# Optimization experiments

Measured on AMD Instinct MI355X. Metric: run time of the kernel, lower is better.

Reference implementation:

```python
import math
import jax, jax.numpy as jnp
import numpy as np

H = 16          # num attention heads
D = 64          # head dim
BUCKETS = 256   # position_buckets
MAX_POS = 512   # max_relative_positions
ATT_SPAN = BUCKETS  # pos_ebd_size A
SCALE_FACTOR = 3    # 1 + len(['c2p','p2c'])


def _log_bucket(rel):
    # log-bucketed relative positions (DeBERTa-v2 _make_log_bucket_position)
    mid = BUCKETS // 2
    rel = jnp.clip(rel, -MAX_POS + 1, MAX_POS - 1)
    sign = jnp.sign(rel).astype(jnp.float32)
    abs_pos = jnp.maximum(jnp.abs(rel), 1)
    log_base = math.log((MAX_POS - 1) / mid)
    log_pos = jnp.ceil(jnp.log(abs_pos.astype(jnp.float32) / mid) / log_base * (mid - 1)) + mid
    bucket = jnp.where(abs_pos < mid, abs_pos.astype(jnp.float32), log_pos) * sign
    return bucket.astype(jnp.int32)


def _rel_pos(q_len, k_len):
    q = jnp.arange(q_len, dtype=jnp.int32)
    k = jnp.arange(k_len, dtype=jnp.int32)
    return _log_bucket(q[:, None] - k[None, :])  # (Q, K)


def setup_inputs() -> dict:
    key = jax.random.key(0)
    ks = jax.random.split(key, 6)
    B, S, Hd = 4, 1024, 1024
    std = 0.02
    return {
        "hidden_states": jax.random.normal(ks[0], (B, S, Hd), jnp.float32),
        "rel_embeddings": jax.random.normal(ks[1], (2 * ATT_SPAN, Hd), jnp.float32) * std,
        "Wq": jax.random.normal(ks[2], (Hd, H * D), jnp.float32) * std,
        "bq": jnp.zeros((H * D,), jnp.float32),
        "Wk": jax.random.normal(ks[3], (Hd, H * D), jnp.float32) * std,
        "bk": jnp.zeros((H * D,), jnp.float32),
        "Wv": jax.random.normal(ks[4], (Hd, H * D), jnp.float32) * std,
        "bv": jnp.zeros((H * D,), jnp.float32),
    }


def reference(hidden_states, rel_embeddings, Wq, bq, Wk, bk, Wv, bv):
    B, S, Hd = hidden_states.shape
    A2 = 2 * ATT_SPAN

    def heads(x):  # (B,S,H*D) -> (B,H,S,D)
        return x.reshape(B, S, H, D).transpose(0, 2, 1, 3)

    q = heads(hidden_states @ Wq + bq)
    k = heads(hidden_states @ Wk + bk)
    v = heads(hidden_states @ Wv + bv)

    scale = math.sqrt(D * SCALE_FACTOR)
    scores = jnp.einsum('bhqd,bhkd->bhqk', q, k) / scale  # (B,H,S,S)

    rel = _rel_pos(S, S)  # (S,S) int32 bucketed relative ids
    # share_att_key=True: pos key/query use key_proj/query_proj
    pos_k = (rel_embeddings @ Wk + bk).reshape(A2, H, D).transpose(1, 0, 2)  # (H,2A,D)
    pos_q = (rel_embeddings @ Wq + bq).reshape(A2, H, D).transpose(1, 0, 2)  # (H,2A,D)

    # c2p: content->position
    c2p = jnp.einsum('bhqd,hkd->bhqk', q, pos_k)  # (B,H,S,2A)
    c2p_idx = jnp.clip(rel + ATT_SPAN, 0, A2 - 1)  # (S,S)
    c2p = jnp.take_along_axis(c2p, jnp.broadcast_to(c2p_idx[None, None], (B, H, S, S)), axis=-1) / scale

    # p2c: position->content
    p2c = jnp.einsum('bhkd,hqd->bhkq', k, pos_q)  # (B,H,S,2A)
    p2c_idx = jnp.clip(-rel + ATT_SPAN, 0, A2 - 1)  # (S,S)
    p2c = jnp.take_along_axis(p2c, jnp.broadcast_to(p2c_idx[None, None], (B, H, S, S)), axis=-1)
    p2c = jnp.swapaxes(p2c, -1, -2) / scale

    probs = jax.nn.softmax(scores + c2p + p2c, axis=-1)
    ctx = jnp.einsum('bhqk,bhkd->bhqd', probs, v)  # (B,H,S,D)
    return ctx.transpose(0, 2, 1, 3).reshape(B, S, H * D)
```

## Files before the change

kernel.cpp:

```cpp
#include <hip/hip_runtime.h>
#include <hip/hip_bf16.h>
#include <math.h>

typedef __attribute__((ext_vector_type(8))) short v8s;
typedef __attribute__((ext_vector_type(4))) short v4sh;
typedef __attribute__((ext_vector_type(4))) unsigned short v4us;
typedef __attribute__((ext_vector_type(4))) float v4f;
typedef __attribute__((ext_vector_type(4))) int   v4i;

#define AS1(p) ((const __attribute__((address_space(1))) void*)(p))
#define AS3(p) ((__attribute__((address_space(3))) void*)(p))

__device__ inline unsigned short f2b(float f){
  __hip_bfloat16 h = __float2bfloat16(f);
  return __builtin_bit_cast(unsigned short, h);
}
__device__ inline float b2f(unsigned short u){
  __hip_bfloat16 h = __builtin_bit_cast(__hip_bfloat16, u);
  return __bfloat162float(h);
}
__device__ inline unsigned cvtpk(float lo, float hi){
  unsigned d;
  asm("v_cvt_pk_bf16_f32 %0, %1, %2" : "=v"(d) : "v"(lo), "v"(hi));
  return d;
}

__device__ inline int bucket_id(int i){
  int r = i - 1023;
  if (r > 511) r = 511; if (r < -511) r = -511;
  float sign = (r > 0) ? 1.f : ((r < 0) ? -1.f : 0.f);
  int ap = r < 0 ? -r : r; if (ap < 1) ap = 1;
  float bucket;
  if (ap < 128) bucket = (float)ap * sign;
  else {
    float lp = ceilf(logf((float)ap / 128.f) / logf(511.f/128.f) * 127.f) + 128.f;
    bucket = lp * sign;
  }
  int idx = (int)bucket + 256;
  if (idx < 0) idx = 0; if (idx > 511) idx = 511;
  return idx;
}

__global__ __launch_bounds__(256) void pack_x(const float* __restrict__ hs,
                                              const float* __restrict__ rel,
                                              const float* __restrict__ Wq,
                                              const float* __restrict__ Wk,
                                              const float* __restrict__ Wv,
                                              unsigned short* __restrict__ X,
                                              unsigned short* __restrict__ Wt3,
                                              short* __restrict__ tab,
                                              unsigned long long* __restrict__ tab64){
  __shared__ unsigned short t[64][65];
  int blk = blockIdx.x;
  if (blk < 2304){
    const int HT8 = 4096*1024/8;
    int i8 = blk*256 + threadIdx.x;
    const float* src = (i8 < HT8) ? (hs + (size_t)i8*8) : (rel + ((size_t)i8 - HT8)*8);
    v8s o;
    #pragma unroll
    for (int j = 0; j < 8; j++) o[j] = (short)f2b(src[j]);
    *(v8s*)&X[(size_t)i8*8] = o;
    return;
  }
  if (blk < 2313){
    int i = (blk - 2304)*256 + threadIdx.x;
    if (i < 2047) tab[i] = (short)bucket_id(i);
    if (i < 2056){
      unsigned long long w = 0;
      #pragma unroll
      for (int r = 0; r < 4; r++)
        w |= (unsigned long long)(unsigned short)bucket_id(i + r) << (16*r);
      tab64[i] = w;
    }
    return;
  }
  int tb = blk - 2313;
  int wsel = tb >> 8, bx = tb & 255;
  const float* in = (wsel == 0) ? Wq : ((wsel == 1) ? Wk : Wv);
  unsigned short* outp = Wt3 + ((size_t)wsel << 20);
  int r0 = (bx >> 4) << 6, c0 = (bx & 15) << 6;
  int tx = threadIdx.x & 63, ty = threadIdx.x >> 6;
  #pragma unroll
  for (int p = 0; p < 16; p++){ int r = (p<<2)+ty; t[tx][r] = f2b(in[(size_t)(r0+r)*1024 + c0+tx]); }
  __syncthreads();
  #pragma unroll
  for (int p = 0; p < 16; p++){ int c = (p<<2)+ty; outp[(size_t)(c0+c)*1024 + r0+tx] = t[c][tx]; }
}

__global__ __launch_bounds__(256) void gemm_qkv(
    const unsigned short* __restrict__ A,
    const unsigned short* __restrict__ Bt3,
    unsigned short* __restrict__ Qa, unsigned short* __restrict__ Ka,
    unsigned short* __restrict__ VtT,
    const float* __restrict__ bq, const float* __restrict__ bk,
    const float* __restrict__ bv, float alpha_q)
{
  __shared__ unsigned short smem[2*128*64];
  unsigned short* a_tile = smem;
  unsigned short* b_tile = smem + 128*64;
  int nb = (blockIdx.x & 7)*108 + (blockIdx.x >> 3);
  int bm = nb / 24, bn = nb % 24;
  int m0 = bm << 7, n0 = bn << 7;
  int tid = threadIdx.x, lane = tid & 63, wave = tid >> 6;
  int l15 = lane & 15, lhi = lane >> 4;
  int rbase = (wave >> 1) << 6, cbase = (wave & 1) << 6;
  int crow[4], csw[4];
  #pragma unroll
  for (int u = 0; u < 4; u++){
    int ch = tid + (u << 8);
    crow[u] = ch >> 3;
    csw[u] = ((ch & 7) ^ (crow[u] & 7)) << 3;
  }
  v4f acc[4][4] = {};
  for (int kt = 0; kt < 1024; kt += 64){
    #pragma unroll
    for (int u = 0; u < 4; u++){
      int ch = tid + (u << 8);
      __builtin_amdgcn_global_load_lds(AS1(A   + (size_t)(m0 + crow[u])*1024 + kt + csw[u]),
                                       AS3(a_tile + (size_t)ch*8), 16, 0, 0);
      __builtin_amdgcn_global_load_lds(AS1(Bt3 + (size_t)(n0 + crow[u])*1024 + kt + csw[u]),
                                       AS3(b_tile + (size_t)ch*8), 16, 0, 0);
    }
    __syncthreads();
    #pragma unroll
    for (int ks = 0; ks < 2; ks++){
      v8s af[4], bfr[4];
      int kb = (ks << 2) + lhi;
      #pragma unroll
      for (int i = 0; i < 4; i++){
        int r = rbase + (i << 4) + l15;
        af[i] = *(const v8s*)&a_tile[r*64 + ((kb ^ (r & 7)) << 3)];
      }
      #pragma unroll
      for (int j = 0; j < 4; j++){
        int r = cbase + (j << 4) + l15;
        bfr[j] = *(const v8s*)&b_tile[r*64 + ((kb ^ (r & 7)) << 3)];
      }
      #pragma unroll
      for (int i = 0; i < 4; i++)
        #pragma unroll
        for (int j = 0; j < 4; j++)
          acc[i][j] = __builtin_amdgcn_mfma_f32_16x16x32_bf16(af[i], bfr[j], acc[i][j], 0, 0, 0);
    }
    __syncthreads();
  }
  int seg = n0 >> 10;
  int nn0 = n0 & 1023;
  if (seg == 2){
    if (m0 >= 4096) return;
    int bb = m0 >> 10, s0 = m0 & 1023;
    #pragma unroll
    for (int i = 0; i < 4; i++){
      int r = rbase + (i << 4) + (lhi << 2);
      #pragma unroll
      for (int j = 0; j < 4; j++){
        int c = cbase + (j << 4) + l15;
        float bvv = bv[nn0 + c];
        #pragma unroll
        for (int rr = 0; rr < 4; rr++)
          smem[c*128 + ((r + rr) ^ ((c & 7) << 4))] = f2b(acc[i][j][rr] + bvv);
      }
    }
    __syncthreads();
    int v = tid >> 3, sc = (tid & 7) << 4;
    #pragma unroll
    for (int vb = 0; vb < 4; vb++){
      int vv = v + (vb << 5);
      #pragma unroll
      for (int c2 = 0; c2 < 2; c2++){
        int sb = sc + (c2 << 3);
        v8s val = *(const v8s*)&smem[vv*128 + (sb ^ ((vv & 7) << 4))];
        *(v8s*)&VtT[((size_t)(bb << 10) + nn0 + vv)*1024 + s0 + sb] = val;
      }
    }
    return;
  }
  unsigned short* C = (seg == 0) ? Qa : Ka;
  const float* bias = (seg == 0) ? bq : bk;
  float alpha = (seg == 0) ? alpha_q : 1.f;
  #pragma unroll
  for (int i = 0; i < 4; i++){
    int row = rbase + (i << 4) + (lhi << 2);
    #pragma unroll
    for (int j = 0; j < 4; j++){
      int col = cbase + (j << 4) + l15;
      float bvv = bias[nn0 + col];
      #pragma unroll
      for (int r = 0; r < 4; r++)
        smem[(row + r)*128 + (col ^ (((row + r) & 7) << 4))] = f2b((acc[i][j][r] + bvv) * alpha);
    }
  }
  __syncthreads();
  #pragma unroll
  for (int c = 0; c < 8; c++){
    int row = (tid >> 4) + (c << 4);
    int col8 = (tid & 15) << 3;
    v8s val = *(const v8s*)&smem[row*128 + (col8 ^ ((row & 7) << 4))];
    *(v8s*)&C[(size_t)(m0 + row)*1024 + nn0 + col8] = val;
  }
}

__global__ __launch_bounds__(256) void gemm_pos(
    const unsigned short* __restrict__ Qa,
    const unsigned short* __restrict__ Ka,
    const short* __restrict__ idxt,
    unsigned short* __restrict__ C2P,
    unsigned short* __restrict__ P2C)
{
  __shared__ unsigned short smem[2*128*64];
  unsigned short* a_tile = smem;
  unsigned short* b_tile = smem + 128*64;
  int xs = (blockIdx.x & 7)*16 + (blockIdx.x >> 3);
  int tab = blockIdx.y >> 4, h = blockIdx.y & 15;
  int bm = xs >> 2, bn = xs & 3;
  int m0 = bm << 7, n0 = bn << 7;
  {
    int s0 = m0 & 1023;
    int lo, hi;
    if (tab == 0){ lo = idxt[s0];       hi = idxt[s0 + 1150]; }
    else         { lo = idxt[896 - s0]; hi = idxt[2046 - s0]; }
    if (n0 > hi + 7 || n0 + 127 < (lo & ~7)) return;
  }
  const unsigned short* A  = tab ? Ka : Qa;
  const unsigned short* Bt = tab ? Qa : Ka;
  unsigned short* C = tab ? P2C : C2P;
  int tid = threadIdx.x, lane = tid & 63, wave = tid >> 6;
  int l15 = lane & 15, lhi = lane >> 4;
  int rbase = (wave >> 1) << 6, cbase = (wave & 1) << 6;
  #pragma unroll
  for (int u = 0; u < 4; u++){
    int ch = tid + (u << 8);
    int row = ch >> 3;
    int csw = ((ch & 7) ^ (row & 7)) << 3;
    __builtin_amdgcn_global_load_lds(AS1(A  + (size_t)(m0 + row)*1024 + (h << 6) + csw),
                                     AS3(a_tile + (size_t)ch*8), 16, 0, 0);
    __builtin_amdgcn_global_load_lds(AS1(Bt + (size_t)(4096 + n0 + row)*1024 + (h << 6) + csw),
                                     AS3(b_tile + (size_t)ch*8), 16, 0, 0);
  }
  __syncthreads();
  v4f acc[4][4] = {};
  #pragma unroll
  for (int ks = 0; ks < 2; ks++){
    v8s af[4], bfr[4];
    int kb = (ks << 2) + lhi;
    #pragma unroll
    for (int i = 0; i < 4; i++){
      int r = rbase + (i << 4) + l15;
      af[i] = *(const v8s*)&a_tile[r*64 + ((kb ^ (r & 7)) << 3)];
    }
    #pragma unroll
    for (int j = 0; j < 4; j++){
      int r = cbase + (j << 4) + l15;
      bfr[j] = *(const v8s*)&b_tile[r*64 + ((kb ^ (r & 7)) << 3)];
    }
    #pragma unroll
    for (int i = 0; i < 4; i++)
      #pragma unroll
      for (int j = 0; j < 4; j++)
        acc[i][j] = __builtin_amdgcn_mfma_f32_16x16x32_bf16(af[i], bfr[j], acc[i][j], 0, 0, 0);
  }
  __syncthreads();
  #pragma unroll
  for (int i = 0; i < 4; i++){
    int row = rbase + (i << 4) + (lhi << 2);
    #pragma unroll
    for (int j = 0; j < 4; j++){
      int col = cbase + (j << 4) + l15;
      #pragma unroll
      for (int r = 0; r < 4; r++)
        smem[(row + r)*128 + (col ^ (((row + r) & 7) << 4))] = f2b(acc[i][j][r]);
    }
  }
  __syncthreads();
  #pragma unroll
  for (int c = 0; c < 8; c++){
    int row = (tid >> 4) + (c << 4);
    int col8 = (tid & 15) << 3;
    v8s val = *(const v8s*)&smem[row*128 + (col8 ^ ((row & 7) << 4))];
    *(v8s*)&C[(size_t)(m0 + row)*8192 + (h << 9) + n0 + col8] = val;
  }
}

__global__ __launch_bounds__(512) void attn(
  const unsigned short* __restrict__ Qall,
  const unsigned short* __restrict__ Kall,
  const unsigned short* __restrict__ Vt,
  const unsigned short* __restrict__ c2p,
  const unsigned short* __restrict__ p2c,
  const short* __restrict__ idxt,
  const unsigned long long* __restrict__ t64g,
  float* __restrict__ out)
{
  __shared__ unsigned short k_lds[64*64];
  __shared__ unsigned short v_lds[2][64*64];
  __shared__ unsigned short cw[128*72];
  __shared__ unsigned short pw[64*152];
  __shared__ short basc[16*128];
  __shared__ short basp[16*64];

  int bid = blockIdx.x;
  int xcd = bid & 7, jj = bid >> 3;
  int bh = (xcd << 3) + (jj >> 3), qb = jj & 7;
  int b = bh >> 4, h = bh & 15;
  int q0 = qb << 7;
  int tid = threadIdx.x, lane = tid & 63, wave = tid >> 6;
  int l15 = lane & 15, lhi = lane >> 4;

  #pragma unroll
  for (int v = 0; v < 6; v++){
    int i = tid + (v << 9);
    if (i < 2048){
      int kt = i >> 7, row = i & 127;
      int bc = idxt[q0 + row - (kt << 6) + 960] & ~7;
      basc[i] = (short)(row*72 - bc);
    } else if (i < 3072){
      int i2 = i - 2048;
      int kt = i2 >> 6, row = i2 & 63;
      int bp = idxt[q0 + 1023 - (kt << 6) - row] & ~7;
      basp[i2] = (short)(row*152 - bp);
    }
  }

  int qrow = q0 + (wave << 4) + l15;
  v8s aq[2];
  #pragma unroll
  for (int ks = 0; ks < 2; ks++)
    aq[ks] = *(const v8s*)&Qall[(size_t)((b << 10) + qrow)*1024 + (h << 6) + (ks << 5) + (lhi << 3)];

  const size_t cbase0 = ((size_t)((b << 10) + q0))*8192 + (h << 9);
  const size_t pbase0 = ((size_t)(b << 10))*8192 + (h << 9);

  unsigned long long t64u[4];

  auto issue_kwin = [&](int kt){
    int k0 = kt << 6;
    {
      int rr = tid >> 3, seg = tid & 7;
      int csw = (seg ^ (rr & 7)) << 3;
      __builtin_amdgcn_global_load_lds(AS1(Kall + (size_t)((b << 10) + k0 + rr)*1024 + (h << 6) + csw),
                                       AS3(k_lds + (size_t)tid*8), 16, 0, 0);
    }
    #pragma unroll
    for (int u = 0; u < 3; u++){
      int pp = tid + (u << 9);
      if (pp < 1152){
        int row = pp / 9, cc = pp - row*9;
        int bc = row*72 - (int)basc[(kt << 7) + row];
        __builtin_amdgcn_global_load_lds(AS1(c2p + cbase0 + (size_t)row*8192 + bc + (cc << 3)),
                                         AS3(cw + (size_t)pp*8), 16, 0, 0);
      }
    }
    #pragma unroll
    for (int u = 0; u < 3; u++){
      int pp = tid + (u << 9);
      if (pp < 1152){
        int row = pp / 18, cc = pp - row*18;
        int bp = row*152 - (int)basp[(kt << 6) + row];
        __builtin_amdgcn_global_load_lds(AS1(p2c + pbase0 + (size_t)(k0 + row)*8192 + bp + (cc << 3)),
                                         AS3(pw + (size_t)(row*152 + (cc << 3))), 16, 0, 0);
      }
    }
  };
  auto issue_tv = [&](int kt, int sel){
    int k0 = kt << 6;
    int Bc = q0 - k0 + (wave << 4) + l15 - (lhi << 2) + 1020;
    #pragma unroll
    for (int j = 0; j < 4; j++) t64u[j] = t64g[Bc - (j << 4)];
    __builtin_amdgcn_sched_barrier(0);
    {
      int rr = tid >> 3, seg = tid & 7;
      int csw = (seg ^ (rr & 7)) << 3;
      __builtin_amdgcn_global_load_lds(AS1(Vt + (size_t)((b << 10) + (h << 6) + rr)*1024 + k0 + csw),
                                       AS3(&v_lds[sel][0] + (size_t)tid*8), 16, 0, 0);
    }
  };

  v4f o_acc[4] = {};
  float m_run = -INFINITY, l_part = 0.f;

  __syncthreads();
  issue_kwin(0);
  __builtin_amdgcn_sched_barrier(0);
  issue_tv(0, 0);

  for (int kt = 0; kt < 16; kt++){
    asm volatile("s_waitcnt vmcnt(5)" ::: "memory");
    __builtin_amdgcn_sched_barrier(0);
    __builtin_amdgcn_s_barrier();
    __builtin_amdgcn_sched_barrier(0);

    v4f s_acc[4] = {};
    __builtin_amdgcn_s_setprio(1);
    #pragma unroll
    for (int j = 0; j < 4; j++){
      int krow = (j << 4) + l15;
      #pragma unroll
      for (int ks = 0; ks < 2; ks++){
        v8s kf = *(const v8s*)&k_lds[krow*64 + ((((ks << 2) + lhi) ^ (krow & 7)) << 3)];
        s_acc[j] = __builtin_amdgcn_mfma_f32_16x16x32_bf16(kf, aq[ks], s_acc[j], 0, 0, 0);
      }
    }
    __builtin_amdgcn_s_setprio(0);
    int cvq = (int)basc[(kt << 7) + (wave << 4) + l15];
    #pragma unroll
    for (int j = 0; j < 4; j++){
      v4sh bp4 = *(const v4sh*)&basp[(kt << 6) + (j << 4) + (lhi << 2)];
      v4us idv = __builtin_bit_cast(v4us, t64u[j]);
      #pragma unroll
      for (int r = 0; r < 4; r++){
        int id = (int)idv[3 - r];
        s_acc[j][r] += b2f(cw[cvq + id]) + b2f(pw[(int)bp4[r] + id]);
      }
    }
    float lmax = s_acc[0][0];
    #pragma unroll
    for (int j = 0; j < 4; j++)
      #pragma unroll
      for (int r = 0; r < 4; r++) lmax = fmaxf(lmax, s_acc[j][r]);
    if (__any(lmax > m_run + 6.f)){
      float mx = lmax;
      mx = fmaxf(mx, __shfl_xor(mx, 16));
      mx = fmaxf(mx, __shfl_xor(mx, 32));
      float mnew = fmaxf(m_run, mx);
      float corr = exp2f(m_run - mnew);
      m_run = mnew;
      l_part *= corr;
      float co[4];
      #pragma unroll
      for (int r = 0; r < 4; r++) co[r] = __shfl(corr, (lhi << 2) + r);
      #pragma unroll
      for (int j = 0; j < 4; j++)
        #pragma unroll
        for (int r = 0; r < 4; r++) o_acc[j][r] *= co[r];
    }
    unsigned wj[4][2];
    float ps = 0.f;
    #pragma unroll
    for (int j = 0; j < 4; j++){
      float p0 = exp2f(s_acc[j][0] - m_run);
      float p1 = exp2f(s_acc[j][1] - m_run);
      float p2 = exp2f(s_acc[j][2] - m_run);
      float p3 = exp2f(s_acc[j][3] - m_run);
      ps += (p0 + p1) + (p2 + p3);
      wj[j][0] = cvtpk(p0, p1);
      wj[j][1] = cvtpk(p2, p3);
    }
    l_part += ps;
    #pragma unroll
    for (int p = 0; p < 2; p++){
      asm("v_permlane32_swap_b32 %0, %1" : "+v"(wj[0][p]), "+v"(wj[1][p]));
      asm("v_permlane32_swap_b32 %0, %1" : "+v"(wj[2][p]), "+v"(wj[3][p]));
      asm("v_permlane16_swap_b32 %0, %1" : "+v"(wj[0][p]), "+v"(wj[1][p]));
      asm("v_permlane16_swap_b32 %0, %1" : "+v"(wj[2][p]), "+v"(wj[3][p]));
    }
    v4i pai0 = { (int)wj[0][0], (int)wj[0][1], (int)wj[1][0], (int)wj[1][1] };
    v4i pai1 = { (int)wj[2][0], (int)wj[2][1], (int)wj[3][0], (int)wj[3][1] };
    v8s pa0 = __builtin_bit_cast(v8s, pai0);
    v8s pa1 = __builtin_bit_cast(v8s, pai1);

    asm volatile("s_waitcnt vmcnt(0)" ::: "memory");
    __builtin_amdgcn_sched_barrier(0);
    __builtin_amdgcn_s_barrier();
    __builtin_amdgcn_sched_barrier(0);

    if (kt < 15){
      issue_kwin(kt + 1);
      __builtin_amdgcn_sched_barrier(0);
      issue_tv(kt + 1, (kt + 1) & 1);
      __builtin_amdgcn_sched_barrier(0);
    }

    const unsigned short* vl = &v_lds[kt & 1][0];
    __builtin_amdgcn_s_setprio(1);
    #pragma unroll
    for (int j = 0; j < 4; j++){
      int vrow = (j << 4) + l15;
      v8s vb0 = *(const v8s*)&vl[vrow*64 + (((lhi) ^ (vrow & 7)) << 3)];
      v8s vb1 = *(const v8s*)&vl[vrow*64 + (((4 + lhi) ^ (vrow & 7)) << 3)];
      o_acc[j] = __builtin_amdgcn_mfma_f32_16x16x32_bf16(pa0, vb0, o_acc[j], 0, 0, 0);
      o_acc[j] = __builtin_amdgcn_mfma_f32_16x16x32_bf16(pa1, vb1, o_acc[j], 0, 0, 0);
    }
    __builtin_amdgcn_s_setprio(0);
  }
  float ls = l_part;
  ls += __shfl_xor(ls, 16);
  ls += __shfl_xor(ls, 32);
  float inv = 1.f / ls;
  float io[4];
  #pragma unroll
  for (int r = 0; r < 4; r++) io[r] = __shfl(inv, (lhi << 2) + r);
  #pragma unroll
  for (int r = 0; r < 4; r++){
    int row = q0 + (wave << 4) + (lhi << 2) + r;
    #pragma unroll
    for (int j = 0; j < 4; j++)
      out[(size_t)((b << 10) + row)*1024 + (h << 6) + (j << 4) + l15] = o_acc[j][r] * io[r];
  }
}

extern "C" void kernel_launch(void* const* d_in, const int* in_sizes, int n_in,
                              void* d_out, int out_size, void* d_ws, size_t ws_size,
                              hipStream_t stream)
{
  const float* hs  = (const float*)d_in[0];
  const float* rel = (const float*)d_in[1];
  const float* Wq  = (const float*)d_in[2];
  const float* bq  = (const float*)d_in[3];
  const float* Wk  = (const float*)d_in[4];
  const float* bk  = (const float*)d_in[5];
  const float* Wv  = (const float*)d_in[6];
  const float* bv  = (const float*)d_in[7];
  float* out = (float*)d_out;

  char* ws = (char*)d_ws;
  size_t off = 0;
  auto alloc = [&](size_t bytes) -> void* {
    void* p = ws + off; off += (bytes + 255) & ~(size_t)255; return p;
  };
  short*              idxt  = (short*)             alloc(2047 * 2);
  unsigned long long* tab64 = (unsigned long long*)alloc(2056 * 8);
  unsigned short* Xb   = (unsigned short*)alloc((size_t)4608*1024*2);
  unsigned short* Wt3  = (unsigned short*)alloc((size_t)3072*1024*2);
  unsigned short* Qa   = (unsigned short*)alloc((size_t)4608*1024*2);
  unsigned short* Ka   = (unsigned short*)alloc((size_t)4608*1024*2);
  unsigned short* VtT  = (unsigned short*)alloc((size_t)4096*1024*2);
  unsigned short* C2P  = (unsigned short*)alloc((size_t)4096*8192*2);
  unsigned short* P2C  = (unsigned short*)alloc((size_t)4096*8192*2);
  (void)                                  alloc(4096);
  (void)ws_size; (void)in_sizes; (void)n_in; (void)out_size;

  pack_x<<<3081, 256, 0, stream>>>(hs, rel, Wq, Wk, Wv, Xb, Wt3, idxt, tab64);

  const float alpha_q = 1.4426950408889634f / sqrtf(192.f);
  gemm_qkv<<<864, 256, 0, stream>>>(Xb, Wt3, Qa, Ka, VtT, bq, bk, bv, alpha_q);

  gemm_pos<<<dim3(128, 32), 256, 0, stream>>>(Qa, Ka, idxt, C2P, P2C);

  attn<<<512, 512, 0, stream>>>(Qa, Ka, VtT, C2P, P2C, idxt, tab64, out);
}
```

Measured before the change: 147.4 us.

## Prefetch c2p/p2c windows into registers and double-buffer K tiles

The c2p/p2c gather windows for the next key tile are now loaded into registers at the start of each iteration, then written to LDS after the bias-add stage behind an extra barrier. The K tile gets its own double buffer and is issued together with V one iteration ahead. This is meant to overlap next-tile global loads with the current tile's QK and softmax work instead of serializing a load phase mid-loop. It costs extra VGPRs for the staged windows at 512 threads per block, an extra barrier per iteration, and a full vmcnt(0) wait at the loop top.

```diff
diff --git a/kernel.cpp b/kernel.cpp
--- a/kernel.cpp
+++ b/kernel.cpp
@@ -291,7 +291,7 @@
   const unsigned long long* __restrict__ t64g,
   float* __restrict__ out)
 {
-  __shared__ unsigned short k_lds[64*64];
+  __shared__ unsigned short k_lds[2][64*64];
   __shared__ unsigned short v_lds[2][64*64];
   __shared__ unsigned short cw[128*72];
   __shared__ unsigned short pw[64*152];
@@ -330,65 +330,85 @@
   const size_t cbase0 = ((size_t)((b << 10) + q0))*8192 + (h << 9);
   const size_t pbase0 = ((size_t)(b << 10))*8192 + (h << 9);
 
+  int rowA[5], ccA[5]; bool cwsel[5], valA[5];
+  #pragma unroll
+  for (int u = 0; u < 5; u++){
+    int pp = tid + (u << 9);
+    valA[u] = pp < 2304;
+    cwsel[u] = pp < 1152;
+    int p2 = cwsel[u] ? pp : (pp - 1152);
+    int dv = cwsel[u] ? (p2 / 9) : (p2 / 18);
+    rowA[u] = dv;
+    ccA[u]  = p2 - dv*(cwsel[u] ? 9 : 18);
+  }
+
+  v8s cwst[5];
   unsigned long long t64u[4];
 
-  auto issue_kwin = [&](int kt){
+  auto issue_win = [&](int kt){
     int k0 = kt << 6;
-    {
-      int rr = tid >> 3, seg = tid & 7;
-      int csw = (seg ^ (rr & 7)) << 3;
-      __builtin_amdgcn_global_load_lds(AS1(Kall + (size_t)((b << 10) + k0 + rr)*1024 + (h << 6) + csw),
-                                       AS3(k_lds + (size_t)tid*8), 16, 0, 0);
-    }
-    #pragma unroll
-    for (int u = 0; u < 3; u++){
-      int pp = tid + (u << 9);
-      if (pp < 1152){
-        int row = pp / 9, cc = pp - row*9;
-        int bc = row*72 - (int)basc[(kt << 7) + row];
-        __builtin_amdgcn_global_load_lds(AS1(c2p + cbase0 + (size_t)row*8192 + bc + (cc << 3)),
-                                         AS3(cw + (size_t)pp*8), 16, 0, 0);
-      }
-    }
-    #pragma unroll
-    for (int u = 0; u < 3; u++){
-      int pp = tid + (u << 9);
-      if (pp < 1152){
-        int row = pp / 18, cc = pp - row*18;
-        int bp = row*152 - (int)basp[(kt << 6) + row];
-        __builtin_amdgcn_global_load_lds(AS1(p2c + pbase0 + (size_t)(k0 + row)*8192 + bp + (cc << 3)),
-                                         AS3(pw + (size_t)(row*152 + (cc << 3))), 16, 0, 0);
+    #pragma unroll
+    for (int u = 0; u < 5; u++){
+      if (valA[u]){
+        if (cwsel[u]){
+          int bc = rowA[u]*72 - (int)basc[(kt << 7) + rowA[u]];
+          cwst[u] = *(const v8s*)&c2p[cbase0 + (size_t)rowA[u]*8192 + bc + (ccA[u] << 3)];
+        } else {
+          int bp = rowA[u]*152 - (int)basp[(kt << 6) + rowA[u]];
+          cwst[u] = *(const v8s*)&p2c[pbase0 + (size_t)(k0 + rowA[u])*8192 + bp + (ccA[u] << 3)];
+        }
       }
     }
   };
-  auto issue_tv = [&](int kt, int sel){
+  auto write_win = [&](){
+    #pragma unroll
+    for (int u = 0; u < 5; u++){
+      if (valA[u]){
+        if (cwsel[u]) *(v8s*)&cw[(size_t)(tid + (u << 9))*8] = cwst[u];
+        else          *(v8s*)&pw[rowA[u]*152 + (ccA[u] << 3)] = cwst[u];
+      }
+    }
+  };
+  auto issue_kv = [&](int kt, int sel){
     int k0 = kt << 6;
-    int Bc = q0 - k0 + (wave << 4) + l15 - (lhi << 2) + 1020;
-    #pragma unroll
-    for (int j = 0; j < 4; j++) t64u[j] = t64g[Bc - (j << 4)];
-    __builtin_amdgcn_sched_barrier(0);
-    {
-      int rr = tid >> 3, seg = tid & 7;
-      int csw = (seg ^ (rr & 7)) << 3;
-      __builtin_amdgcn_global_load_lds(AS1(Vt + (size_t)((b << 10) + (h << 6) + rr)*1024 + k0 + csw),
-                                       AS3(&v_lds[sel][0] + (size_t)tid*8), 16, 0, 0);
-    }
+    int rr = tid >> 3, seg = tid & 7;
+    int csw = (seg ^ (rr & 7)) << 3;
+    __builtin_amdgcn_global_load_lds(AS1(Kall + (size_t)((b << 10) + k0 + rr)*1024 + (h << 6) + csw),
+                                     AS3(&k_lds[sel][0] + (size_t)tid*8), 16, 0, 0);
+    __builtin_amdgcn_global_load_lds(AS1(Vt + (size_t)((b << 10) + (h << 6) + rr)*1024 + k0 + csw),
+                                     AS3(&v_lds[sel][0] + (size_t)tid*8), 16, 0, 0);
   };
 
   v4f o_acc[4] = {};
   float m_run = -INFINITY, l_part = 0.f;
 
   __syncthreads();
-  issue_kwin(0);
+  issue_win(0);
   __builtin_amdgcn_sched_barrier(0);
-  issue_tv(0, 0);
+  issue_kv(0, 0);
+  __builtin_amdgcn_sched_barrier(0);
+  write_win();
+  __builtin_amdgcn_sched_barrier(0);
 
   for (int kt = 0; kt < 16; kt++){
-    asm volatile("s_waitcnt vmcnt(5)" ::: "memory");
+    int k0 = kt << 6;
+    asm volatile("s_waitcnt vmcnt(0) lgkmcnt(0)" ::: "memory");
     __builtin_amdgcn_sched_barrier(0);
     __builtin_amdgcn_s_barrier();
     __builtin_amdgcn_sched_barrier(0);
 
+    {
+      int Bc = q0 - k0 + (wave << 4) + l15 - (lhi << 2) + 1020;
+      #pragma unroll
+      for (int j = 0; j < 4; j++) t64u[j] = t64g[Bc - (j << 4)];
+    }
+    if (kt < 15){
+      issue_win(kt + 1);
+      issue_kv(kt + 1, (kt + 1) & 1);
+    }
+    __builtin_amdgcn_sched_barrier(0);
+
+    const unsigned short* kl = &k_lds[kt & 1][0];
     v4f s_acc[4] = {};
     __builtin_amdgcn_s_setprio(1);
     #pragma unroll
@@ -396,7 +416,7 @@
       int krow = (j << 4) + l15;
       #pragma unroll
       for (int ks = 0; ks < 2; ks++){
-        v8s kf = *(const v8s*)&k_lds[krow*64 + ((((ks << 2) + lhi) ^ (krow & 7)) << 3)];
+        v8s kf = *(const v8s*)&kl[krow*64 + ((((ks << 2) + lhi) ^ (krow & 7)) << 3)];
         s_acc[j] = __builtin_amdgcn_mfma_f32_16x16x32_bf16(kf, aq[ks], s_acc[j], 0, 0, 0);
       }
     }
@@ -412,6 +432,13 @@
         s_acc[j][r] += b2f(cw[cvq + id]) + b2f(pw[(int)bp4[r] + id]);
       }
     }
+
+    __builtin_amdgcn_sched_barrier(0);
+    __builtin_amdgcn_s_barrier();
+    __builtin_amdgcn_sched_barrier(0);
+    if (kt < 15) write_win();
+    __builtin_amdgcn_sched_barrier(0);
+
     float lmax = s_acc[0][0];
     #pragma unroll
     for (int j = 0; j < 4; j++)
@@ -457,18 +484,6 @@
     v4i pai1 = { (int)wj[2][0], (int)wj[2][1], (int)wj[3][0], (int)wj[3][1] };
     v8s pa0 = __builtin_bit_cast(v8s, pai0);
     v8s pa1 = __builtin_bit_cast(v8s, pai1);
-
-    asm volatile("s_waitcnt vmcnt(0)" ::: "memory");
-    __builtin_amdgcn_sched_barrier(0);
-    __builtin_amdgcn_s_barrier();
-    __builtin_amdgcn_sched_barrier(0);
-
-    if (kt < 15){
-      issue_kwin(kt + 1);
-      __builtin_amdgcn_sched_barrier(0);
-      issue_tv(kt + 1, (kt + 1) & 1);
-      __builtin_amdgcn_sched_barrier(0);
-    }
 
     const unsigned short* vl = &v_lds[kt & 1][0];
     __builtin_amdgcn_s_setprio(1);
```

Measured after the change: 178.3 us. 20.9% more time.
